# Kernel optimization log

Measured on AMD Instinct MI355X. Metric: run time of the kernel, lower is better.

## Reference

```python
import jax, jax.numpy as jnp
import numpy as np

SIZE = 5           # kernel size and num_rbfs
MUL = 16           # multiplicity of 0e and 1o in irreps_in/out
CROP = SIZE // 2
# e3nn FullyConnectedTensorProduct path weights (normalization='component', path_normalization='element'):
# path_weight = sqrt((2*l_out+1) / fan_in), fan_in = sum over paths into that output of mul1*mul2.
# out 0e: paths (0e,0e)+(1o,1o) -> fan_in=32; out 1o: paths (0e,1o)+(1o,0e) -> fan_in=32.
PW0 = (1.0 / 32.0) ** 0.5          # scalar output paths
PW1 = (3.0 / 32.0) ** 0.5          # vector output paths
INV_SQRT3 = 3.0 ** -0.5            # wigner-3j values: w3j(1,0,1)=w3j(0,1,1)=w3j(1,1,0)=delta/sqrt(3)


def _lattice_consts():
    # lattice of kernel offsets, steps=(1,1,1) keeps all SIZE points per axis
    r = jnp.linspace(-1.0, 1.0, SIZE)
    lat = jnp.stack(jnp.meshgrid(r, r, r, indexing='ij'), axis=-1)   # [5,5,5,3]
    d = jnp.linalg.norm(lat, axis=-1)                                # [5,5,5]
    # soft_one_hot_linspace(basis='smooth_finite', endpoint=True) over [0,1] with SIZE bins
    values = jnp.linspace(0.0, 1.0, SIZE)
    step = values[1] - values[0]
    diff = (d[..., None] - values) / step                            # [5,5,5,5]
    def sus(t):  # soft unit step: exp(-1/t) for t>0 else 0
        return jnp.where(t > 0, jnp.exp(-1.0 / jnp.where(t > 0, t, 1.0)), 0.0)
    emb = 1.14136 * np.float32(np.e ** 2) * sus(diff + 1.0) * sus(1.0 - diff)
    # spherical harmonics lmax=1, normalize=True, 'component' normalization
    n = lat / jnp.maximum(d, 1e-12)[..., None]                       # zero vector -> 0 (like F.normalize)
    sh0 = jnp.ones_like(d)                                           # l=0 component-normalized
    sh1 = (3.0 ** 0.5) * n                                           # l=1 component-normalized, [5,5,5,3]
    return emb, sh0, sh1


def _make_kernel(weight):
    """emb @ weight -> per-voxel TP weights; tp.right(sh, w) -> [5,5,5,in=64,out=64] kernel."""
    emb, sh0, sh1 = _lattice_consts()
    w = emb @ weight                                                 # [5,5,5,1024]
    S = w.shape[:3]
    blk = MUL * MUL
    # path order: (0e,0e->0e), (0e,1o->1o), (1o,0e->1o), (1o,1o->0e)
    w1, w2, w3, w4 = [w[..., i * blk:(i + 1) * blk].reshape(*S, MUL, MUL) for i in range(4)]
    k_ss = PW0 * w1 * sh0[..., None, None]                           # [s,u,w]   scalar in -> scalar out
    k_sv = PW1 * INV_SQRT3 * jnp.einsum('...uw,...k->...uwk', w2, sh1)   # [s,u,w,k] scalar in -> vector out
    k_vs = PW0 * INV_SQRT3 * jnp.einsum('...uw,...i->...uiw', w4, sh1)   # [s,u,i,w] vector in -> scalar out
    eye3 = jnp.eye(3, dtype=w.dtype)
    k_vv = PW1 * INV_SQRT3 * (w3 * sh0[..., None, None])[..., :, None, :, None] \
           * eye3[None, None, None, None, :, None, :]                # [s,u,i,w,k] vector in -> vector out
    top = jnp.concatenate([k_ss, k_sv.reshape(*S, MUL, 3 * MUL)], axis=-1)            # [s,16,64]
    bot = jnp.concatenate([k_vs.reshape(*S, 3 * MUL, MUL),
                           k_vv.reshape(*S, 3 * MUL, 3 * MUL)], axis=-1)              # [s,48,64]
    kernel = jnp.concatenate([top, bot], axis=-2)                    # [5,5,5,in,out]
    return jnp.transpose(kernel, (4, 3, 0, 1, 2))                    # 'xyzio->oixyz'


def reference(x, weight, w_sc0, w_sc1):
    B = x.shape[0]
    sp = x.shape[2:]
    # self-connection: e3nn Linear (per-irrep mixing, 1/sqrt(fan_in) norm), then crop
    xs = x[:, :MUL]                                                  # scalars [B,16,X,Y,Z]
    xv = x[:, MUL:].reshape(B, MUL, 3, *sp)                          # vectors [B,16,3,X,Y,Z]
    inv = 1.0 / MUL ** 0.5
    sc_s = jnp.einsum('buxyz,uw->bwxyz', xs, w_sc0) * inv
    sc_v = (jnp.einsum('buixyz,uw->bwixyz', xv, w_sc1) * inv).reshape(B, 3 * MUL, *sp)
    sc = jnp.concatenate([sc_s, sc_v], axis=1)[:, :, CROP:-CROP, CROP:-CROP, CROP:-CROP]
    # equivariant kernel + dense conv3d (torch conv3d = correlation = VALID conv here)
    kernel = _make_kernel(weight)                                    # [64,64,5,5,5]
    conv = jax.lax.conv_general_dilated(x, kernel, (1, 1, 1), 'VALID',
                                        dimension_numbers=('NCDHW', 'OIDHW', 'NCDHW'))
    return sc + conv


def setup_inputs() -> dict:
    key = jax.random.key(0)
    k1, k2, k3, k4 = jax.random.split(key, 4)
    weight_numel = 4 * MUL * MUL  # 1024
    return {
        'x': jax.random.normal(k1, (1, 4 * MUL, 56, 56, 56), dtype=jnp.float32),
        'weight': jax.random.normal(k2, (SIZE, weight_numel), dtype=jnp.float32)
                  * np.float32((2.0 / weight_numel) ** 0.5),  # kaiming_normal(relu)
        'w_sc0': jax.random.normal(k3, (MUL, MUL), dtype=jnp.float32),
        'w_sc1': jax.random.normal(k4, (MUL, MUL), dtype=jnp.float32),
    }
```

## Files before the change

kernel.cpp:

```cpp
#include <hip/hip_runtime.h>
#include <hip/hip_bf16.h>

typedef unsigned short ush;
typedef __bf16 v8bf __attribute__((ext_vector_type(8)));
typedef float f32x4 __attribute__((ext_vector_type(4)));
typedef float f32x16 __attribute__((ext_vector_type(16)));

#define SPD 56
#define OSD 52
#define SP3 175616
#define N_A_ELEMS (2*125*64*32)
#define NCX 5488
#define NBA 2008

__global__ void aux_kernel(const float* __restrict__ x, ush* __restrict__ xb,
                           const float* __restrict__ weight, const float* __restrict__ w_sc0,
                           const float* __restrict__ w_sc1, ush* __restrict__ A) {
    __shared__ float t[64 * 33];
    const int bid = blockIdx.x;
    const int tid = threadIdx.x;
    if (bid < NCX) {
        const int s0 = (bid % 2744) * 64;
        const int cg = bid / 2744;
        const int w = tid >> 6, l = tid & 63;
        #pragma unroll
        for (int k = 0; k < 8; k++) {
            int c = w * 8 + k;
            t[l * 33 + c] = x[(cg * 32 + c) * SP3 + s0 + l];
        }
        __syncthreads();
        int v = tid >> 2, qq = tid & 3;
        union { ush u[8]; uint4 q4; } pk;
        #pragma unroll
        for (int j = 0; j < 8; j++) {
            __hip_bfloat16 b = __float2bfloat16(t[v * 33 + qq * 8 + j]);
            pk.u[j] = *(ush*)&b;
        }
        *(uint4*)(xb + ((size_t)(cg * SP3 + s0 + v)) * 32 + qq * 8) = pk.q4;
        return;
    }
    int f = (bid - NCX) * 256 + tid;
    if (f >= N_A_ELEMS) {
        if (f < N_A_ELEMS + 2048) A[f] = 0;
        return;
    }
    int c   = f & 31;
    int o   = (f >> 5) & 63;
    int t2  = f >> 11;
    int tau = t2 % 125;
    int cg  = t2 / 125;
    int i   = cg * 32 + c;
    int dz = tau / 25, dy = (tau / 5) % 5, dx = tau % 5;
    float rz = -1.f + 0.5f * dz, ry = -1.f + 0.5f * dy, rx = -1.f + 0.5f * dx;
    float d = sqrtf(rz * rz + ry * ry + rx * rx);
    float dm = fmaxf(d, 1e-12f);
    float nv[3] = { rz / dm, ry / dm, rx / dm };
    float emb[5];
    #pragma unroll
    for (int m = 0; m < 5; m++) {
        float diff = 4.f * d - (float)m;
        float ta = diff + 1.f, tb = 1.f - diff;
        float sa = ta > 0.f ? expf(-1.f / ta) : 0.f;
        float sb = tb > 0.f ? expf(-1.f / tb) : 0.f;
        emb[m] = 1.14136f * 7.3890560989306495f * sa * sb;
    }
    const float PW0 = 0.17677669529663687f;
    const float PW1 = 0.30618621784789724f;
    const float IS3 = 0.57735026918962576f;
    float val = 0.f;
    int widx = -1; float scale = 0.f;
    if (i < 16) {
        if (o < 16) { widx = i * 16 + o;                         scale = PW0; }
        else        { int wc = (o - 16) / 3, kc = (o - 16) % 3;
                      widx = 256 + i * 16 + wc;                  scale = PW1 * nv[kc]; }
    } else {
        int u = (i - 16) / 3, ic = (i - 16) % 3;
        if (o < 16) { widx = 768 + u * 16 + o;                   scale = PW0 * nv[ic]; }
        else        { int wc = (o - 16) / 3, jc = (o - 16) % 3;
                      if (ic == jc) { widx = 512 + u * 16 + wc;  scale = PW1 * IS3; } }
    }
    if (widx >= 0) {
        float wv = 0.f;
        #pragma unroll
        for (int m = 0; m < 5; m++) wv += emb[m] * weight[m * 1024 + widx];
        val = scale * wv;
    }
    if (tau == 62) {
        if (i < 16 && o < 16) val += 0.25f * w_sc0[i * 16 + o];
        else if (i >= 16 && o >= 16) {
            int u = (i - 16) / 3, ic = (i - 16) % 3;
            int wc = (o - 16) / 3, jc = (o - 16) % 3;
            if (ic == jc) val += 0.25f * w_sc1[u * 16 + wc];
        }
    }
    __hip_bfloat16 b = __float2bfloat16(val);
    A[f] = *(ush*)&b;
}

__launch_bounds__(256, 2)
__global__ void conv_main(const ush* __restrict__ A, const ush* __restrict__ xb,
                          float* __restrict__ out) {
    __shared__ ush patch[32768];

    const int b  = blockIdx.x;
    const int bp = (b & 7) * 148 + (b >> 3);
    if (bp >= 1183) return;
    const int bx = bp % 13;
    const int t1 = bp / 13;
    const int by = t1 % 13;
    const int bz = t1 / 13;
    const int x0 = bx * 4, y0 = by * 4;
    const int z0 = (bz == 6) ? 44 : bz * 8;

    const int tid  = threadIdx.x;
    const int wv   = tid >> 6;
    const int lane = tid & 63;
    const int lhi  = lane >> 5;
    const int rbase32 = ((lane >> 4) & 1) * 64 + ((lane >> 2) & 3) * 8 + (lane & 3);
    const ush* Aw = A + (lane & 31) * 32 + lhi * 8;

    f32x16 acc[2][4];
    #pragma unroll
    for (int mt = 0; mt < 2; mt++)
        #pragma unroll
        for (int nt = 0; nt < 4; nt++)
            acc[mt][nt] = (f32x16)(0.f);

    for (int cg = 0; cg < 2; cg++) {
        __syncthreads();
        #pragma unroll 4
        for (int it = 0; it < 12; it++) {
            int u   = tid + it * 256;
            int qq  = u & 3;
            int vox = u >> 2;
            int xp = vox & 7, yp = (vox >> 3) & 7, zp = vox >> 6;
            const ush* g = xb + ((size_t)((cg * SPD + z0 + zp) * SPD + (y0 + yp)) * SPD + (x0 + xp)) * 32 + qq * 8;
            uint4 v = *(const uint4*)g;
            int slot = vox * 4 + ((qq + vox + (vox >> 3)) & 3);
            *(uint4*)(patch + slot * 8) = v;
        }
        __syncthreads();

        const int t0 = wv * 32;
        int dz = t0 / 25; int rr = t0 - dz * 25; int dy = rr / 5; int dx = rr - dy * 5;

        #pragma unroll 2
        for (int j = 0; j < 32; j++) {
            int t = t0 + j;
            int vb = dz * 64 + dy * 8 + dx;
            if (vb > 292) vb = 0;
            int v0 = vb + rbase32;
            int pre = v0 + (v0 >> 3);
            int slot0 = v0 * 4 + ((lhi + pre) & 3);
            int slot1 = v0 * 4 + ((2 + lhi + pre) & 3);

            v8bf bf[4][2];
            #pragma unroll
            for (int nt = 0; nt < 4; nt++) {
                bf[nt][0] = *(const v8bf*)(patch + slot0 * 8 + nt * 4096);
                bf[nt][1] = *(const v8bf*)(patch + slot1 * 8 + nt * 4096);
            }

            int toff = (t < 125) ? (cg * 125 + t) : 250;
            v8bf af[2][2];
            #pragma unroll
            for (int mt = 0; mt < 2; mt++)
                #pragma unroll
                for (int h = 0; h < 2; h++)
                    af[mt][h] = *(const v8bf*)(Aw + (size_t)toff * 2048 + mt * 1024 + h * 16);

            #pragma unroll
            for (int h = 0; h < 2; h++)
                #pragma unroll
                for (int mt = 0; mt < 2; mt++)
                    #pragma unroll
                    for (int nt = 0; nt < 4; nt++)
                        acc[mt][nt] = __builtin_amdgcn_mfma_f32_32x32x16_bf16(af[mt][h], bf[nt][h], acc[mt][nt], 0, 0, 0);

            int c1 = (dx == 4);
            dx = c1 ? 0 : dx + 1;
            int c2 = c1 & (dy == 4);
            dy = c2 ? 0 : dy + c1;
            dz += c2;
        }
    }

    __syncthreads();
    float* red = (float*)patch;
    if (wv >= 2) {
        #pragma unroll
        for (int mt = 0; mt < 2; mt++)
            #pragma unroll
            for (int nt = 0; nt < 4; nt++) {
                float* p = red + (wv - 2) * 8192 + (mt * 4 + nt) * 1024 + lane * 16;
                #pragma unroll
                for (int s = 0; s < 4; s++) {
                    f32x4 v = { acc[mt][nt][s*4+0], acc[mt][nt][s*4+1], acc[mt][nt][s*4+2], acc[mt][nt][s*4+3] };
                    *(f32x4*)(p + s * 4) = v;
                }
            }
    }
    __syncthreads();
    if (wv < 2) {
        #pragma unroll
        for (int mt = 0; mt < 2; mt++)
            #pragma unroll
            for (int nt = 0; nt < 4; nt++) {
                float* p = red + wv * 8192 + (mt * 4 + nt) * 1024 + lane * 16;
                #pragma unroll
                for (int s = 0; s < 4; s++) {
                    f32x4 v = *(const f32x4*)(p + s * 4);
                    f32x4 m = { acc[mt][nt][s*4+0], acc[mt][nt][s*4+1], acc[mt][nt][s*4+2], acc[mt][nt][s*4+3] };
                    *(f32x4*)(p + s * 4) = v + m;
                }
            }
    }
    __syncthreads();

    const int yy = y0 + ((lane >> 2) & 3);
    const int xx = x0 + (lane & 3);
    #pragma unroll
    for (int k = 0; k < 2; k++) {
        int fi = wv * 2 + k;
        int mt = fi >> 2, nt = fi & 3;
        int zz = z0 + nt * 2 + ((lane >> 4) & 1);
        #pragma unroll
        for (int s = 0; s < 4; s++) {
            f32x4 v = *(const f32x4*)(red + fi * 1024 + lane * 16 + s * 4);
            v += *(const f32x4*)(red + 8192 + fi * 1024 + lane * 16 + s * 4);
            #pragma unroll
            for (int e = 0; e < 4; e++) {
                int o = mt * 32 + e + 8 * s + 4 * lhi;
                out[((o * OSD + zz) * OSD + yy) * OSD + xx] = v[e];
            }
        }
    }
}

extern "C" void kernel_launch(void* const* d_in, const int* in_sizes, int n_in,
                              void* d_out, int out_size, void* d_ws, size_t ws_size,
                              hipStream_t stream) {
    const float* x      = (const float*)d_in[0];
    const float* weight = (const float*)d_in[1];
    const float* w_sc0  = (const float*)d_in[2];
    const float* w_sc1  = (const float*)d_in[3];
    float* out = (float*)d_out;

    ush* A  = (ush*)d_ws;
    ush* xb = (ush*)((char*)d_ws + (2 << 20));

    aux_kernel<<<NCX + NBA, 256, 0, stream>>>(x, xb, weight, w_sc0, w_sc1, A);
    conv_main<<<1184, 256, 0, stream>>>(A, xb, out);
}
```

Before: 234.4 us.

## Software-pipeline A and patch fragment loads across taps in conv MFMA loop

Restructures the inner tap loop into an explicitly double-buffered pipeline. The global loads of A fragments for the next tap and the LDS loads of B fragments for the next half-step are issued before the MFMAs on the current data, so their latency is meant to hide behind matrix work. The A weight layout is padded to 128 taps per channel group with zeroed tail rows, which removes the per-tap bounds select and allows plain pointer increments. The cost is more live registers and an extra prefetch past the last tap, which the padding covers.

```diff
diff --git a/kernel.cpp b/kernel.cpp
--- a/kernel.cpp
+++ b/kernel.cpp
@@ -9,9 +9,9 @@
 #define SPD 56
 #define OSD 52
 #define SP3 175616
-#define N_A_ELEMS (2*125*64*32)
 #define NCX 5488
-#define NBA 2008
+#define NBA 2112
+#define N_A_ELEMS (264*2048)
 
 __global__ void aux_kernel(const float* __restrict__ x, ush* __restrict__ xb,
                            const float* __restrict__ weight, const float* __restrict__ w_sc0,
@@ -40,15 +40,13 @@
         return;
     }
     int f = (bid - NCX) * 256 + tid;
-    if (f >= N_A_ELEMS) {
-        if (f < N_A_ELEMS + 2048) A[f] = 0;
-        return;
-    }
+    if (f >= N_A_ELEMS) return;
     int c   = f & 31;
     int o   = (f >> 5) & 63;
-    int t2  = f >> 11;
-    int tau = t2 % 125;
-    int cg  = t2 / 125;
+    int T   = f >> 11;
+    int cg  = (T >= 128) ? 1 : 0;
+    int tau = T - cg * 128;
+    if (tau >= 125) { A[f] = 0; return; }
     int i   = cg * 32 + c;
     int dz = tau / 25, dy = (tau / 5) % 5, dx = tau % 5;
     float rz = -1.f + 0.5f * dz, ry = -1.f + 0.5f * dy, rx = -1.f + 0.5f * dx;
@@ -117,7 +115,7 @@
     const int lane = tid & 63;
     const int lhi  = lane >> 5;
     const int rbase32 = ((lane >> 4) & 1) * 64 + ((lane >> 2) & 3) * 8 + (lane & 3);
-    const ush* Aw = A + (lane & 31) * 32 + lhi * 8;
+    const int t0 = wv * 32;
 
     f32x16 acc[2][4];
     #pragma unroll
@@ -126,7 +124,55 @@
         for (int nt = 0; nt < 4; nt++)
             acc[mt][nt] = (f32x16)(0.f);
 
+    int dz, dy, dx;
+    v8bf afA[2][2], afB[2][2], bfc[4], bfn[4];
+
+    auto SLOTS = [&](int& s0, int& s1) {
+        int vb = dz * 64 + dy * 8 + dx;
+        if (vb > 292) vb = 0;
+        int v0 = vb + rbase32;
+        int pre = v0 + (v0 >> 3);
+        s0 = v0 * 4 + ((lhi + pre) & 3);
+        s1 = v0 * 4 + ((2 + lhi + pre) & 3);
+    };
+    auto ADV = [&]() {
+        int c1 = (dx == 4);
+        dx = c1 ? 0 : dx + 1;
+        int c2 = c1 & (dy == 4);
+        dy = c2 ? 0 : dy + c1;
+        dz += c2;
+    };
+    auto LDB = [&](v8bf (&bf)[4], int slot) {
+        #pragma unroll
+        for (int nt = 0; nt < 4; nt++)
+            bf[nt] = *(const v8bf*)(patch + slot * 8 + nt * 4096);
+    };
+    auto LDA = [&](v8bf (&af)[2][2], const ush* p) {
+        #pragma unroll
+        for (int mt = 0; mt < 2; mt++)
+            #pragma unroll
+            for (int h = 0; h < 2; h++)
+                af[mt][h] = *(const v8bf*)(p + mt * 1024 + h * 16);
+    };
+    auto MM0 = [&](v8bf (&af)[2][2], v8bf (&bf)[4]) {
+        #pragma unroll
+        for (int mt = 0; mt < 2; mt++)
+            #pragma unroll
+            for (int nt = 0; nt < 4; nt++)
+                acc[mt][nt] = __builtin_amdgcn_mfma_f32_32x32x16_bf16(af[mt][0], bf[nt], acc[mt][nt], 0, 0, 0);
+    };
+    auto MM1 = [&](v8bf (&af)[2][2], v8bf (&bf)[4]) {
+        #pragma unroll
+        for (int mt = 0; mt < 2; mt++)
+            #pragma unroll
+            for (int nt = 0; nt < 4; nt++)
+                acc[mt][nt] = __builtin_amdgcn_mfma_f32_32x32x16_bf16(af[mt][1], bf[nt], acc[mt][nt], 0, 0, 0);
+    };
+
     for (int cg = 0; cg < 2; cg++) {
+        const ush* Ap = A + ((size_t)(cg * 128 + t0)) * 2048 + (lane & 31) * 32 + lhi * 8;
+        LDA(afA, Ap);
+
         __syncthreads();
         #pragma unroll 4
         for (int it = 0; it < 12; it++) {
@@ -141,47 +187,29 @@
         }
         __syncthreads();
 
-        const int t0 = wv * 32;
-        int dz = t0 / 25; int rr = t0 - dz * 25; int dy = rr / 5; int dx = rr - dy * 5;
-
-        #pragma unroll 2
-        for (int j = 0; j < 32; j++) {
-            int t = t0 + j;
-            int vb = dz * 64 + dy * 8 + dx;
-            if (vb > 292) vb = 0;
-            int v0 = vb + rbase32;
-            int pre = v0 + (v0 >> 3);
-            int slot0 = v0 * 4 + ((lhi + pre) & 3);
-            int slot1 = v0 * 4 + ((2 + lhi + pre) & 3);
-
-            v8bf bf[4][2];
-            #pragma unroll
-            for (int nt = 0; nt < 4; nt++) {
-                bf[nt][0] = *(const v8bf*)(patch + slot0 * 8 + nt * 4096);
-                bf[nt][1] = *(const v8bf*)(patch + slot1 * 8 + nt * 4096);
-            }
-
-            int toff = (t < 125) ? (cg * 125 + t) : 250;
-            v8bf af[2][2];
-            #pragma unroll
-            for (int mt = 0; mt < 2; mt++)
-                #pragma unroll
-                for (int h = 0; h < 2; h++)
-                    af[mt][h] = *(const v8bf*)(Aw + (size_t)toff * 2048 + mt * 1024 + h * 16);
-
-            #pragma unroll
-            for (int h = 0; h < 2; h++)
-                #pragma unroll
-                for (int mt = 0; mt < 2; mt++)
-                    #pragma unroll
-                    for (int nt = 0; nt < 4; nt++)
-                        acc[mt][nt] = __builtin_amdgcn_mfma_f32_32x32x16_bf16(af[mt][h], bf[nt][h], acc[mt][nt], 0, 0, 0);
-
-            int c1 = (dx == 4);
-            dx = c1 ? 0 : dx + 1;
-            int c2 = c1 & (dy == 4);
-            dy = c2 ? 0 : dy + c1;
-            dz += c2;
+        dz = t0 / 25; int rr = t0 - dz * 25; dy = rr / 5; dx = rr - dy * 5;
+        int s0, s1, s1c;
+        SLOTS(s0, s1);
+        LDB(bfc, s0);
+        s1c = s1;
+        ADV();
+
+        #pragma unroll 1
+        for (int j = 0; j < 32; j += 2) {
+            LDA(afB, Ap + 2048);
+            LDB(bfn, s1c);
+            MM0(afA, bfc);
+            SLOTS(s0, s1);
+            LDB(bfc, s0);
+            MM1(afA, bfn);
+            s1c = s1; ADV(); Ap += 2048;
+            LDA(afA, Ap + 2048);
+            LDB(bfn, s1c);
+            MM0(afB, bfc);
+            SLOTS(s0, s1);
+            LDB(bfc, s0);
+            MM1(afB, bfn);
+            s1c = s1; ADV(); Ap += 2048;
         }
     }
 
```

New measurement: 232.6 us. No clear change (-0.8%).

## Split conv waves across tap halves and N halves to raise occupancy

Applied to the files above, without the earlier changes.

Repartitions the four waves in each conv block. Each pair of waves now takes half of the 128 padded kernel taps, and within a pair each wave takes half of the output voxel tiles, so the per-wave accumulator shrinks from eight 32x32 tiles to four. The weight buffer is padded to 128 taps per channel group with zeros, which removes the per-tap clamping. With fewer registers and smaller LDS the kernel allows three blocks per CU instead of two, and the cross-wave reduction drops to a single LDS round that writes output directly. The cost is less A-fragment reuse per MFMA, so global and L2 load traffic for weights per wave goes up.

```diff
diff --git a/kernel.cpp b/kernel.cpp
--- a/kernel.cpp
+++ b/kernel.cpp
@@ -9,9 +9,9 @@
 #define SPD 56
 #define OSD 52
 #define SP3 175616
-#define N_A_ELEMS (2*125*64*32)
 #define NCX 5488
-#define NBA 2008
+#define NBA 2112
+#define N_A_ELEMS (264*2048)
 
 __global__ void aux_kernel(const float* __restrict__ x, ush* __restrict__ xb,
                            const float* __restrict__ weight, const float* __restrict__ w_sc0,
@@ -40,15 +40,13 @@
         return;
     }
     int f = (bid - NCX) * 256 + tid;
-    if (f >= N_A_ELEMS) {
-        if (f < N_A_ELEMS + 2048) A[f] = 0;
-        return;
-    }
+    if (f >= N_A_ELEMS) return;
     int c   = f & 31;
     int o   = (f >> 5) & 63;
-    int t2  = f >> 11;
-    int tau = t2 % 125;
-    int cg  = t2 / 125;
+    int T   = f >> 11;
+    int cg  = (T >= 128) ? 1 : 0;
+    int tau = T - cg * 128;
+    if (tau >= 125) { A[f] = 0; return; }
     int i   = cg * 32 + c;
     int dz = tau / 25, dy = (tau / 5) % 5, dx = tau % 5;
     float rz = -1.f + 0.5f * dz, ry = -1.f + 0.5f * dy, rx = -1.f + 0.5f * dx;
@@ -97,10 +95,10 @@
     A[f] = *(ush*)&b;
 }
 
-__launch_bounds__(256, 2)
+__launch_bounds__(256, 3)
 __global__ void conv_main(const ush* __restrict__ A, const ush* __restrict__ xb,
                           float* __restrict__ out) {
-    __shared__ ush patch[32768];
+    __shared__ ush patch[24576];
 
     const int b  = blockIdx.x;
     const int bp = (b & 7) * 148 + (b >> 3);
@@ -116,15 +114,17 @@
     const int wv   = tid >> 6;
     const int lane = tid & 63;
     const int lhi  = lane >> 5;
+    const int th   = wv >> 1;
+    const int np   = wv & 1;
     const int rbase32 = ((lane >> 4) & 1) * 64 + ((lane >> 2) & 3) * 8 + (lane & 3);
-    const ush* Aw = A + (lane & 31) * 32 + lhi * 8;
-
-    f32x16 acc[2][4];
+    const int t0 = th * 64;
+
+    f32x16 acc[2][2];
     #pragma unroll
     for (int mt = 0; mt < 2; mt++)
         #pragma unroll
-        for (int nt = 0; nt < 4; nt++)
-            acc[mt][nt] = (f32x16)(0.f);
+        for (int k = 0; k < 2; k++)
+            acc[mt][k] = (f32x16)(0.f);
 
     for (int cg = 0; cg < 2; cg++) {
         __syncthreads();
@@ -141,99 +141,87 @@
         }
         __syncthreads();
 
-        const int t0 = wv * 32;
         int dz = t0 / 25; int rr = t0 - dz * 25; int dy = rr / 5; int dx = rr - dy * 5;
+        const ush* Ap = A + ((size_t)(cg * 128 + t0)) * 2048 + (lane & 31) * 32 + lhi * 8;
+        const ush* Bp = patch + np * 8192;
 
         #pragma unroll 2
-        for (int j = 0; j < 32; j++) {
-            int t = t0 + j;
+        for (int j = 0; j < 64; j++) {
             int vb = dz * 64 + dy * 8 + dx;
             if (vb > 292) vb = 0;
             int v0 = vb + rbase32;
             int pre = v0 + (v0 >> 3);
-            int slot0 = v0 * 4 + ((lhi + pre) & 3);
-            int slot1 = v0 * 4 + ((2 + lhi + pre) & 3);
-
-            v8bf bf[4][2];
-            #pragma unroll
-            for (int nt = 0; nt < 4; nt++) {
-                bf[nt][0] = *(const v8bf*)(patch + slot0 * 8 + nt * 4096);
-                bf[nt][1] = *(const v8bf*)(patch + slot1 * 8 + nt * 4096);
+            int s0 = v0 * 4 + ((lhi + pre) & 3);
+            int s1 = v0 * 4 + ((2 + lhi + pre) & 3);
+
+            v8bf bf[2][2];
+            #pragma unroll
+            for (int k = 0; k < 2; k++) {
+                bf[k][0] = *(const v8bf*)(Bp + s0 * 8 + k * 4096);
+                bf[k][1] = *(const v8bf*)(Bp + s1 * 8 + k * 4096);
             }
-
-            int toff = (t < 125) ? (cg * 125 + t) : 250;
             v8bf af[2][2];
             #pragma unroll
             for (int mt = 0; mt < 2; mt++)
                 #pragma unroll
                 for (int h = 0; h < 2; h++)
-                    af[mt][h] = *(const v8bf*)(Aw + (size_t)toff * 2048 + mt * 1024 + h * 16);
+                    af[mt][h] = *(const v8bf*)(Ap + mt * 1024 + h * 16);
 
             #pragma unroll
             for (int h = 0; h < 2; h++)
                 #pragma unroll
                 for (int mt = 0; mt < 2; mt++)
                     #pragma unroll
-                    for (int nt = 0; nt < 4; nt++)
-                        acc[mt][nt] = __builtin_amdgcn_mfma_f32_32x32x16_bf16(af[mt][h], bf[nt][h], acc[mt][nt], 0, 0, 0);
+                    for (int k = 0; k < 2; k++)
+                        acc[mt][k] = __builtin_amdgcn_mfma_f32_32x32x16_bf16(af[mt][h], bf[k][h], acc[mt][k], 0, 0, 0);
 
             int c1 = (dx == 4);
             dx = c1 ? 0 : dx + 1;
             int c2 = c1 & (dy == 4);
             dy = c2 ? 0 : dy + c1;
             dz += c2;
+            Ap += 2048;
         }
     }
 
     __syncthreads();
     float* red = (float*)patch;
-    if (wv >= 2) {
+    const int yy = y0 + ((lane >> 2) & 3);
+    const int xx = x0 + (lane & 3);
+    if (th == 1) {
         #pragma unroll
         for (int mt = 0; mt < 2; mt++)
             #pragma unroll
-            for (int nt = 0; nt < 4; nt++) {
-                float* p = red + (wv - 2) * 8192 + (mt * 4 + nt) * 1024 + lane * 16;
+            for (int k = 0; k < 2; k++) {
+                float* p = red + np * 4096 + (mt * 2 + k) * 1024 + lane * 16;
                 #pragma unroll
                 for (int s = 0; s < 4; s++) {
-                    f32x4 v = { acc[mt][nt][s*4+0], acc[mt][nt][s*4+1], acc[mt][nt][s*4+2], acc[mt][nt][s*4+3] };
+                    f32x4 v = { acc[mt][k][s*4+0], acc[mt][k][s*4+1], acc[mt][k][s*4+2], acc[mt][k][s*4+3] };
                     *(f32x4*)(p + s * 4) = v;
                 }
             }
     }
     __syncthreads();
-    if (wv < 2) {
+    if (th == 0) {
         #pragma unroll
         for (int mt = 0; mt < 2; mt++)
             #pragma unroll
-            for (int nt = 0; nt < 4; nt++) {
-                float* p = red + wv * 8192 + (mt * 4 + nt) * 1024 + lane * 16;
+            for (int k = 0; k < 2; k++) {
+                const float* p = red + np * 4096 + (mt * 2 + k) * 1024 + lane * 16;
+                int nt = np * 2 + k;
+                int zz = z0 + nt * 2 + ((lane >> 4) & 1);
                 #pragma unroll
                 for (int s = 0; s < 4; s++) {
                     f32x4 v = *(const f32x4*)(p + s * 4);
-                    f32x4 m = { acc[mt][nt][s*4+0], acc[mt][nt][s*4+1], acc[mt][nt][s*4+2], acc[mt][nt][s*4+3] };
-                    *(f32x4*)(p + s * 4) = v + m;
+                    f32x4 m = { acc[mt][k][s*4+0], acc[mt][k][s*4+1], acc[mt][k][s*4+2], acc[mt][k][s*4+3] };
+                    v += m;
+                    #pragma unroll
+                    for (int e = 0; e < 4; e++) {
+                        int o = mt * 32 + e + 8 * s + 4 * lhi;
+                        out[((o * OSD + zz) * OSD + yy) * OSD + xx] = v[e];
+                    }
                 }
             }
-    }
-    __syncthreads();
-
-    const int yy = y0 + ((lane >> 2) & 3);
-    const int xx = x0 + (lane & 3);
-    #pragma unroll
-    for (int k = 0; k < 2; k++) {
-        int fi = wv * 2 + k;
-        int mt = fi >> 2, nt = fi & 3;
-        int zz = z0 + nt * 2 + ((lane >> 4) & 1);
-        #pragma unroll
-        for (int s = 0; s < 4; s++) {
-            f32x4 v = *(const f32x4*)(red + fi * 1024 + lane * 16 + s * 4);
-            v += *(const f32x4*)(red + 8192 + fi * 1024 + lane * 16 + s * 4);
-            #pragma unroll
-            for (int e = 0; e < 4; e++) {
-                int o = mt * 32 + e + 8 * s + 4 * lhi;
-                out[((o * OSD + zz) * OSD + yy) * OSD + xx] = v[e];
-            }
-        }
     }
 }
 
```

After: 267.9 us. +14.3%, slower.
